# Kernel optimization log

Hardware: AMD Instinct MI355X
Metric: run time of the kernel (lower is better)

## Reference

```python
import jax, jax.numpy as jnp
import numpy as np

N = 50000      # nodes
E = 800000     # edges
F_NODE = 64
PE = 16
F_EDGE = 16
H = 128        # hidden_dim
L = 4          # num_layers
G = 64         # graphs in batch
NC = 10        # num_classes
BN_EPS = 1e-5


def _bn(h, g, b):
    # BatchNorm1d with batch statistics (deterministic train-style stats, no dropout)
    m = jnp.mean(h, axis=0)
    v = jnp.var(h, axis=0)
    return (h - m) * jax.lax.rsqrt(v + BN_EPS) * g + b


def setup_inputs() -> dict:
    key = jax.random.key(0)
    ks = jax.random.split(key, 16)
    p = lambda k, shape: (jax.random.normal(k, shape, jnp.float32) * 0.05)
    return dict(
        x=jax.random.normal(ks[0], (N, F_NODE), jnp.float32),
        pe=jax.random.normal(ks[1], (N, PE), jnp.float32),
        edge_index=jax.random.randint(ks[2], (2, E), 0, N),
        edge_attr=jax.random.normal(ks[3], (E, F_EDGE), jnp.float32),
        batch=jnp.sort(jax.random.randint(ks[4], (N,), 0, G)),
        W_in=p(ks[5], (F_NODE + PE, H)), b_in=jnp.zeros((H,), jnp.float32),
        We_edge=p(ks[6], (L, F_EDGE, H)), be_edge=jnp.zeros((L, H), jnp.float32),
        eps=jnp.zeros((L,), jnp.float32),
        W1_gin=p(ks[7], (L, H, 2 * H)), b1_gin=jnp.zeros((L, 2 * H), jnp.float32),
        W2_gin=p(ks[8], (L, 2 * H, H)), b2_gin=jnp.zeros((L, H), jnp.float32),
        bn1_g=jnp.ones((L, H), jnp.float32), bn1_b=jnp.zeros((L, H), jnp.float32),
        W1_ffn=p(ks[9], (L, H, 2 * H)), b1_ffn=jnp.zeros((L, 2 * H), jnp.float32),
        W2_ffn=p(ks[10], (L, 2 * H, H)), b2_ffn=jnp.zeros((L, H), jnp.float32),
        bn2_g=jnp.ones((L, H), jnp.float32), bn2_b=jnp.zeros((L, H), jnp.float32),
        W_r1=p(ks[11], (H, H)), b_r1=jnp.zeros((H,), jnp.float32),
        W_r2=p(ks[12], (H, NC)), b_r2=jnp.zeros((NC,), jnp.float32),
    )


def reference(x, pe, edge_index, edge_attr, batch,
              W_in, b_in, We_edge, be_edge, eps,
              W1_gin, b1_gin, W2_gin, b2_gin, bn1_g, bn1_b,
              W1_ffn, b1_ffn, W2_ffn, b2_ffn, bn2_g, bn2_b,
              W_r1, b_r1, W_r2, b_r2):
    src, dst = edge_index[0], edge_index[1]  # PyG: row=source j, col=target i
    # input projection on [x || pe]
    h = jax.nn.relu(jnp.concatenate([x, pe], axis=-1) @ W_in + b_in)  # [N,H]
    for l in range(L):
        # --- GINEConv: msg = relu(x_j + lin_edge(e_ij)); sum-aggregate to target
        e = edge_attr @ We_edge[l] + be_edge[l]                        # [E,H]
        msg = jax.nn.relu(h[src] + e)                                  # gather + fuse
        agg = jax.ops.segment_sum(msg, dst, num_segments=N)           # scatter-add
        z = (1.0 + eps[l]) * h + agg
        z = jax.nn.relu(z @ W1_gin[l] + b1_gin[l]) @ W2_gin[l] + b2_gin[l]
        # --- GNNPlusLayer: BN -> ReLU -> residual (identity proj, in==out)
        z = jax.nn.relu(_bn(z, bn1_g[l], bn1_b[l]))
        z = z + h
        # --- FFN (eval mode): out = lin2(relu(lin1(z))) + z, then BN
        f = jax.nn.relu(z @ W1_ffn[l] + b1_ffn[l]) @ W2_ffn[l] + b2_ffn[l]
        h = _bn(f + z, bn2_g[l], bn2_b[l])
    # --- global mean pool over graphs
    sums = jax.ops.segment_sum(h, batch, num_segments=G)               # [G,H]
    counts = jax.ops.segment_sum(jnp.ones((N,), h.dtype), batch, num_segments=G)
    hg = sums / jnp.maximum(counts, 1.0)[:, None]
    # --- readout MLP (dropout off in eval)
    return jax.nn.relu(hg @ W_r1 + b_r1) @ W_r2 + b_r2                 # [G,NC]
```

## Files before the change

kernel.cpp:

```cpp
#include <hip/hip_runtime.h>
#include <hip/hip_bf16.h>

#define NN 50000
#define NE 800000
#define FIN 80
#define H 128
#define H2 256
#define NG 64
#define NCLS 10
#define BN_EPS 1e-5f
#define NB 196
#define LDK 40
#define LDY 264

typedef __attribute__((ext_vector_type(8))) short bf16x8;
typedef __attribute__((ext_vector_type(8))) unsigned short us8;
typedef __attribute__((ext_vector_type(4))) float f32x4;
typedef __attribute__((ext_vector_type(2))) float f32x2;

__device__ __forceinline__ unsigned short f2b(float f) {
    __hip_bfloat16 h = __float2bfloat16(f);
    return *(unsigned short*)&h;
}
__device__ __forceinline__ float b2f(unsigned short u) {
    unsigned v = (unsigned)u << 16;
    return __uint_as_float(v);
}

__global__ void wprep_all(const float* __restrict__ W1g, const float* __restrict__ W2g,
                          const float* __restrict__ W1f, const float* __restrict__ W2f,
                          unsigned short* __restrict__ wt)
{
    const int idx = blockIdx.x * 256 + threadIdx.x;
    const int m = idx >> 17;
    const int r = idx & 131071;
    const float* W;
    unsigned short* Wt;
    int K, Nn;
    if (m == 0)      { W = W1g; Wt = wt;              K = 128; Nn = 256; }
    else if (m == 1) { W = W2g; Wt = wt + 4 * 65536;  K = 256; Nn = 128; }
    else if (m == 2) { W = W1f; Wt = wt + 8 * 65536;  K = 128; Nn = 256; }
    else             { W = W2f; Wt = wt + 12 * 65536; K = 256; Nn = 128; }
    const int per = K * Nn;
    const int l = r / per;
    const int rr = r - l * per;
    const int k = rr / Nn;
    const int n = rr - k * Nn;
    const float wv = W[r];
    const unsigned short hi = f2b(wv);
    const unsigned short lo = f2b(wv - b2f(hi));
    const int KB = K >> 5;
    const int kb = k >> 5, kk = k & 31;
    unsigned short* base = Wt + (size_t)l * 2 * per;
    base[((size_t)(0 * KB + kb) * Nn + n) * 32 + kk] = hi;
    base[((size_t)(1 * KB + kb) * Nn + n) * 32 + kk] = lo;
}

template<bool ZF>
__global__ __launch_bounds__(256, 2)
void gemm_pair(const void* __restrict__ Ap, const float* __restrict__ hres,
               const unsigned short* __restrict__ Wt1, const unsigned short* __restrict__ Wt2,
               const float* __restrict__ b1, const float* __restrict__ b2,
               const float* __restrict__ statsIn, const float* __restrict__ bng,
               const float* __restrict__ bnb, float* __restrict__ statsOut,
               float* __restrict__ Cout, float inv_n, int M)
{
    __shared__ unsigned short sA[ZF ? 128 : 1][LDK];
    __shared__ unsigned short sy[128][LDY];
    __shared__ float sAB[128];
    __shared__ float sSH[128];

    const int tid = threadIdx.x;
    const int m0 = blockIdx.x * 128;
    const int lane = tid & 63;
    const int w = tid >> 6;
    const int fr = lane & 15;
    const int fq = (lane >> 4) * 8;
    const int crow4 = (lane >> 4) * 4;

    if (ZF) {
#pragma unroll
        for (int rep = 0; rep < 2; ++rep) {
            const int c = lane + rep * 64;
            float su = 0.f, qu = 0.f;
#pragma unroll
            for (int s = 0; s < 8; ++s) {
                su += statsIn[s * 256 + c];
                qu += statsIn[s * 256 + 128 + c];
            }
            const float mean = su * inv_n;
            const float var = qu * inv_n - mean * mean;
            const float a = bng[c] * rsqrtf(var + BN_EPS);
            sAB[c] = a;
            sSH[c] = fmaf(-mean, a, bnb[c]);
        }
    }

    f32x4 acc1[2][16];
#pragma unroll
    for (int r = 0; r < 2; ++r)
#pragma unroll
        for (int c = 0; c < 16; ++c) acc1[r][c] = (f32x4)(0.f);

    const int arow = tid >> 1;
    const int akh = (tid & 1) * 16;
    const int gm = m0 + arow;

    for (int kb = 0; kb < 4; ++kb) {
        bf16x8 a0, a1;
        if (ZF) {
            if (gm < M) {
                const float* tf = (const float*)Ap + (size_t)gm * 128 + kb * 32 + akh;
                const float* hf = hres + (size_t)gm * 128 + kb * 32 + akh;
                const float4 t0 = *(const float4*)tf;
                const float4 t1 = *(const float4*)(tf + 4);
                const float4 t2 = *(const float4*)(tf + 8);
                const float4 t3 = *(const float4*)(tf + 12);
                const float4 h0 = *(const float4*)hf;
                const float4 h1 = *(const float4*)(hf + 4);
                const float4 h2 = *(const float4*)(hf + 8);
                const float4 h3 = *(const float4*)(hf + 12);
                const float tv[16] = {t0.x, t0.y, t0.z, t0.w, t1.x, t1.y, t1.z, t1.w,
                                      t2.x, t2.y, t2.z, t2.w, t3.x, t3.y, t3.z, t3.w};
                const float hv[16] = {h0.x, h0.y, h0.z, h0.w, h1.x, h1.y, h1.z, h1.w,
                                      h2.x, h2.y, h2.z, h2.w, h3.x, h3.y, h3.z, h3.w};
                us8 p0, p1;
#pragma unroll
                for (int i = 0; i < 8; ++i) {
                    const int c = kb * 32 + akh + i;
                    const int c2 = c + 8;
                    p0[i] = f2b(fmaxf(fmaf(tv[i], sAB[c], sSH[c]), 0.f) + hv[i]);
                    p1[i] = f2b(fmaxf(fmaf(tv[8 + i], sAB[c2], sSH[c2]), 0.f) + hv[8 + i]);
                }
                *(us8*)&sA[arow][akh]     = p0;
                *(us8*)&sA[arow][akh + 8] = p1;
            } else {
                *(float4*)&sA[arow][akh]     = make_float4(0.f, 0.f, 0.f, 0.f);
                *(float4*)&sA[arow][akh + 8] = make_float4(0.f, 0.f, 0.f, 0.f);
            }
            a0 = *(const bf16x8*)&sA[w * 32 + fr][kb * 32 + akh - akh + fq];
            a0 = *(const bf16x8*)&sA[w * 32 + fr][fq];
            a1 = *(const bf16x8*)&sA[w * 32 + 16 + fr][fq];
        } else {
            const unsigned short* z0 = (const unsigned short*)Ap +
                                       (size_t)(m0 + w * 32 + fr) * 128 + kb * 32 + fq;
            const unsigned short* z1 = (const unsigned short*)Ap +
                                       (size_t)(m0 + w * 32 + 16 + fr) * 128 + kb * 32 + fq;
            a0 = *(const bf16x8*)z0;
            a1 = *(const bf16x8*)z1;
        }
#pragma unroll
        for (int nt = 0; nt < 16; ++nt) {
            const bf16x8 bh = *(const bf16x8*)&Wt1[((size_t)(kb) * 256 + nt * 16 + fr) * 32 + fq];
            const bf16x8 bl = *(const bf16x8*)&Wt1[((size_t)(4 + kb) * 256 + nt * 16 + fr) * 32 + fq];
            acc1[0][nt] = __builtin_amdgcn_mfma_f32_16x16x32_bf16(a0, bh, acc1[0][nt], 0, 0, 0);
            acc1[0][nt] = __builtin_amdgcn_mfma_f32_16x16x32_bf16(a0, bl, acc1[0][nt], 0, 0, 0);
            acc1[1][nt] = __builtin_amdgcn_mfma_f32_16x16x32_bf16(a1, bh, acc1[1][nt], 0, 0, 0);
            acc1[1][nt] = __builtin_amdgcn_mfma_f32_16x16x32_bf16(a1, bl, acc1[1][nt], 0, 0, 0);
        }
    }

#pragma unroll
    for (int nt = 0; nt < 16; ++nt) {
        const float bb = b1[nt * 16 + fr];
#pragma unroll
        for (int r = 0; r < 2; ++r) {
            const int row0 = w * 32 + r * 16 + crow4;
#pragma unroll
            for (int reg = 0; reg < 4; ++reg) {
                const float o = fmaxf(acc1[r][nt][reg] + bb, 0.f);
                sy[row0 + reg][nt * 16 + fr] = f2b(o);
            }
        }
    }

    f32x4 acc2[2][8];
#pragma unroll
    for (int r = 0; r < 2; ++r)
#pragma unroll
        for (int c = 0; c < 8; ++c) acc2[r][c] = (f32x4)(0.f);

    for (int kb = 0; kb < 8; ++kb) {
        const bf16x8 ya0 = *(const bf16x8*)&sy[w * 32 + fr][kb * 32 + fq];
        const bf16x8 ya1 = *(const bf16x8*)&sy[w * 32 + 16 + fr][kb * 32 + fq];
#pragma unroll
        for (int ct = 0; ct < 8; ++ct) {
            const bf16x8 bh = *(const bf16x8*)&Wt2[((size_t)(kb) * 128 + ct * 16 + fr) * 32 + fq];
            const bf16x8 bl = *(const bf16x8*)&Wt2[((size_t)(8 + kb) * 128 + ct * 16 + fr) * 32 + fq];
            acc2[0][ct] = __builtin_amdgcn_mfma_f32_16x16x32_bf16(ya0, bh, acc2[0][ct], 0, 0, 0);
            acc2[0][ct] = __builtin_amdgcn_mfma_f32_16x16x32_bf16(ya0, bl, acc2[0][ct], 0, 0, 0);
            acc2[1][ct] = __builtin_amdgcn_mfma_f32_16x16x32_bf16(ya1, bh, acc2[1][ct], 0, 0, 0);
            acc2[1][ct] = __builtin_amdgcn_mfma_f32_16x16x32_bf16(ya1, bl, acc2[1][ct], 0, 0, 0);
        }
    }

    float s[8], q[8];
#pragma unroll
    for (int c = 0; c < 8; ++c) { s[c] = 0.f; q[c] = 0.f; }
#pragma unroll
    for (int r = 0; r < 2; ++r) {
        const int rbase = m0 + w * 32 + r * 16 + crow4;
#pragma unroll
        for (int ct = 0; ct < 8; ++ct) {
            const int gc = ct * 16 + fr;
            const float bb = b2[gc];
#pragma unroll
            for (int reg = 0; reg < 4; ++reg) {
                const int gr = rbase + reg;
                if (gr >= M) continue;
                float o = acc2[r][ct][reg] + bb;
                if (ZF) {
                    const float tv = ((const float*)Ap)[(size_t)gr * 128 + gc];
                    const float hv = hres[(size_t)gr * 128 + gc];
                    o += fmaxf(fmaf(tv, sAB[gc], sSH[gc]), 0.f) + hv;
                }
                s[ct] += o;
                q[ct] = fmaf(o, o, q[ct]);
                Cout[(size_t)gr * 128 + gc] = o;
            }
        }
    }

#pragma unroll
    for (int c = 0; c < 8; ++c) {
        s[c] += __shfl_xor(s[c], 32, 64); s[c] += __shfl_xor(s[c], 16, 64);
        q[c] += __shfl_xor(q[c], 32, 64); q[c] += __shfl_xor(q[c], 16, 64);
    }
    __syncthreads();
    float* red = (float*)sy;
    if (lane < 16) {
#pragma unroll
        for (int c = 0; c < 8; ++c) {
            red[w * 128 + c * 16 + lane]       = s[c];
            red[512 + w * 128 + c * 16 + lane] = q[c];
        }
    }
    __syncthreads();
    if (tid < 128) {
        const float ss = red[tid] + red[128 + tid] + red[256 + tid] + red[384 + tid];
        const float qq = red[512 + tid] + red[640 + tid] + red[768 + tid] + red[896 + tid];
        float* slab = statsOut + (blockIdx.x & 7) * 256;
        atomicAdd(&slab[tid], ss);
        atomicAdd(&slab[128 + tid], qq);
    }
}

__global__ __launch_bounds__(256, 4)
void inproj_kernel(const float* __restrict__ x, const float* __restrict__ pe,
                   const float* __restrict__ W, const float* __restrict__ bias,
                   float* __restrict__ C, unsigned short* __restrict__ Cb, int M)
{
    __shared__ float aT[16][129];
    __shared__ float wsh[16][129];

    const int tid = threadIdx.x;
    const int m0 = blockIdx.x * 128;
    const int rm = (tid >> 4) * 8;
    const int rn = (tid & 15) * 8;

    float acc[8][8];
#pragma unroll
    for (int i = 0; i < 8; ++i)
#pragma unroll
        for (int j = 0; j < 8; ++j) acc[i][j] = 0.f;

    const int lm = tid & 127;
    const int kq = (tid >> 7) * 8;
    const int wk = tid >> 4;
    const int wj = (tid & 15) * 8;

    for (int k0 = 0; k0 < FIN; k0 += 16) {
        {
            const int gm = m0 + lm;
            const int c = k0 + kq;
            if (gm < M) {
                const float* srcp = (c < 64) ? (x + (size_t)gm * 64 + c)
                                             : (pe + (size_t)gm * 16 + (c - 64));
                const float4 v0 = *(const float4*)srcp;
                const float4 v1 = *(const float4*)(srcp + 4);
                aT[kq + 0][lm] = v0.x; aT[kq + 1][lm] = v0.y;
                aT[kq + 2][lm] = v0.z; aT[kq + 3][lm] = v0.w;
                aT[kq + 4][lm] = v1.x; aT[kq + 5][lm] = v1.y;
                aT[kq + 6][lm] = v1.z; aT[kq + 7][lm] = v1.w;
            } else {
#pragma unroll
                for (int i = 0; i < 8; ++i) aT[kq + i][lm] = 0.f;
            }
        }
        {
#pragma unroll
            for (int j = 0; j < 8; ++j)
                wsh[wk][wj + j] = W[(size_t)(k0 + wk) * H + wj + j];
        }
        __syncthreads();
#pragma unroll
        for (int k = 0; k < 16; ++k) {
            const float av[8] = {aT[k][rm], aT[k][rm + 1], aT[k][rm + 2], aT[k][rm + 3],
                                 aT[k][rm + 4], aT[k][rm + 5], aT[k][rm + 6], aT[k][rm + 7]};
            const float bv[8] = {wsh[k][rn], wsh[k][rn + 1], wsh[k][rn + 2], wsh[k][rn + 3],
                                 wsh[k][rn + 4], wsh[k][rn + 5], wsh[k][rn + 6], wsh[k][rn + 7]};
#pragma unroll
            for (int i = 0; i < 8; ++i)
#pragma unroll
                for (int j = 0; j < 8; ++j)
                    acc[i][j] = fmaf(av[i], bv[j], acc[i][j]);
        }
        __syncthreads();
    }

    float bv[8];
#pragma unroll
    for (int j = 0; j < 8; ++j) bv[j] = bias[rn + j];
#pragma unroll
    for (int i = 0; i < 8; ++i) {
        const int gm = m0 + rm + i;
        if (gm >= M) continue;
        float o[8];
#pragma unroll
        for (int j = 0; j < 8; ++j) o[j] = fmaxf(acc[i][j] + bv[j], 0.f);
        *(float4*)&C[(size_t)gm * H + rn]     = make_float4(o[0], o[1], o[2], o[3]);
        *(float4*)&C[(size_t)gm * H + rn + 4] = make_float4(o[4], o[5], o[6], o[7]);
        us8 pk;
#pragma unroll
        for (int j = 0; j < 8; ++j) pk[j] = f2b(o[j]);
        *(us8*)&Cb[(size_t)gm * H + rn] = pk;
    }
}

__global__ void hist_kernel(const int* __restrict__ ei, int* __restrict__ deg)
{
    const int e = blockIdx.x * 256 + threadIdx.x;
    if (e < NE) atomicAdd(&deg[ei[NE + e]], 1);
}

__global__ void bsum_kernel(const int* __restrict__ deg, int* __restrict__ bsum)
{
    const int tid = threadIdx.x;
    const int i = blockIdx.x * 256 + tid;
    int v = (i < NN) ? deg[i] : 0;
#pragma unroll
    for (int off = 32; off > 0; off >>= 1) v += __shfl_down(v, off, 64);
    __shared__ int ws[4];
    if ((tid & 63) == 0) ws[tid >> 6] = v;
    __syncthreads();
    if (tid == 0) bsum[blockIdx.x] = ws[0] + ws[1] + ws[2] + ws[3];
}

__global__ void bscan_kernel(int* __restrict__ bsum)
{
    __shared__ int sh[256];
    const int tid = threadIdx.x;
    sh[tid] = (tid < NB) ? bsum[tid] : 0;
    __syncthreads();
    for (int off = 1; off < 256; off <<= 1) {
        const int t = (tid >= off) ? sh[tid - off] : 0;
        __syncthreads();
        sh[tid] += t;
        __syncthreads();
    }
    if (tid < NB) bsum[tid] = (tid == 0) ? 0 : sh[tid - 1];
}

__global__ void bwrite_kernel(const int* __restrict__ deg, const int* __restrict__ boff,
                              int* __restrict__ rowptr, int* __restrict__ cursor)
{
    __shared__ int sh[256];
    const int tid = threadIdx.x;
    const int i = blockIdx.x * 256 + tid;
    const int v = (i < NN) ? deg[i] : 0;
    sh[tid] = v;
    __syncthreads();
    for (int off = 1; off < 256; off <<= 1) {
        const int t = (tid >= off) ? sh[tid - off] : 0;
        __syncthreads();
        sh[tid] += t;
        __syncthreads();
    }
    if (i < NN) {
        const int pos = boff[blockIdx.x] + sh[tid] - v;
        rowptr[i] = pos;
        cursor[i] = pos;
    }
    if (blockIdx.x == 0 && tid == 0) rowptr[NN] = NE;
}

__global__ void scat_idx(const int* __restrict__ ei, int* __restrict__ cursor,
                         int* __restrict__ src_s, int* __restrict__ perm)
{
    const int e = blockIdx.x * 256 + threadIdx.x;
    if (e >= NE) return;
    const int pos = atomicAdd(&cursor[ei[NE + e]], 1);
    src_s[pos] = ei[e];
    perm[pos] = e;
}

__global__ void gather_ea(const float* __restrict__ ea, const int* __restrict__ perm,
                          float* __restrict__ ea_s)
{
    const int idx = blockIdx.x * 256 + threadIdx.x;
    const int pos = idx >> 2;
    const int qd = idx & 3;
    const int e = perm[pos];
    *(float4*)&ea_s[(size_t)pos * 16 + qd * 4] = *(const float4*)&ea[(size_t)e * 16 + qd * 4];
}

__global__ __launch_bounds__(256)
void agg_kernel(const float* __restrict__ h, const unsigned short* __restrict__ hb,
                const int* __restrict__ rowptr, const int* __restrict__ src_s,
                const float* __restrict__ ea_s, const float* __restrict__ We,
                const float* __restrict__ be, const float* __restrict__ eps, int l,
                unsigned short* __restrict__ zb)
{
    const int lane = threadIdx.x & 63;
    const int w = threadIdx.x >> 6;
    const int n = blockIdx.x * 4 + w;
    if (n >= NN) return;

    f32x2 wv[16];
#pragma unroll
    for (int k = 0; k < 16; ++k)
        wv[k] = *(const f32x2*)&We[k * H + 2 * lane];
    const f32x2 bev = *(const f32x2*)&be[2 * lane];

    const int beg = __builtin_amdgcn_readfirstlane(rowptr[n]);
    const int end = __builtin_amdgcn_readfirstlane(rowptr[n + 1]);

    const float e1 = 1.0f + eps[l];
    f32x2 acc = (*(const f32x2*)&h[(size_t)n * H + 2 * lane]) * e1;

    for (int i0 = beg; i0 < end; i0 += 16) {
        const int jn = min(16, end - i0);
        int srcs[16];
#pragma unroll
        for (int j = 0; j < 16; ++j)
            srcs[j] = src_s[(i0 + j < end) ? (i0 + j) : (end - 1)];
        unsigned hraw[16];
#pragma unroll
        for (int j = 0; j < 16; ++j)
            hraw[j] = *(const unsigned*)&hb[(size_t)srcs[j] * H + 2 * lane];
#pragma unroll
        for (int j = 0; j < 16; ++j) {
            if (j >= jn) break;
            const float* ar = ea_s + (size_t)(i0 + j) * 16;
            f32x2 s2 = bev;
#pragma unroll
            for (int k = 0; k < 16; ++k)
                s2 = __builtin_elementwise_fma((f32x2)(ar[k]), wv[k], s2);
            f32x2 hv = {__uint_as_float(hraw[j] << 16),
                        __uint_as_float(hraw[j] & 0xffff0000u)};
            f32x2 m = hv + s2;
            m = __builtin_elementwise_max(m, (f32x2)(0.f));
            acc += m;
        }
    }
    const unsigned u = ((unsigned)f2b(acc[1]) << 16) | (unsigned)f2b(acc[0]);
    *(unsigned*)&zb[(size_t)n * H + 2 * lane] = u;
}

__global__ void bn_apply_kernel(const float* __restrict__ u, const float* __restrict__ st,
                                const float* __restrict__ g, const float* __restrict__ b,
                                float* __restrict__ h, unsigned short* __restrict__ hb,
                                float inv_n)
{
    const int i = blockIdx.x * 256 + threadIdx.x;
    const int c = i & (H - 1);
    float su = 0.f, qu = 0.f;
#pragma unroll
    for (int s = 0; s < 8; ++s) { su += st[s * 256 + c]; qu += st[s * 256 + 128 + c]; }
    const float mean = su * inv_n;
    const float var = qu * inv_n - mean * mean;
    const float a = g[c] * rsqrtf(var + BN_EPS);
    const float sh = fmaf(-mean, a, b[c]);
    const float v = fmaf(u[i], a, sh);
    h[i] = v;
    hb[i] = f2b(v);
}

__global__ void pool_kernel(const float* __restrict__ h, const int* __restrict__ batch,
                            float* __restrict__ pool, float* __restrict__ cnt, int n)
{
    const int c = threadIdx.x & (H - 1);
    const int half = threadIdx.x >> 7;
    const int r0 = blockIdx.x * 256 + half * 128;
    if (r0 >= n) return;
    const int rend = min(r0 + 128, n);
    int gprev = batch[r0];
    float acc = 0.f;
    int run = 0;
    for (int r = r0; r < rend; ++r) {
        const int g = batch[r];
        if (g != gprev) {
            atomicAdd(&pool[gprev * H + c], acc);
            if (c == 0) atomicAdd(&cnt[gprev], (float)run);
            acc = 0.f; run = 0; gprev = g;
        }
        acc += h[(size_t)r * H + c];
        run++;
    }
    atomicAdd(&pool[gprev * H + c], acc);
    if (c == 0) atomicAdd(&cnt[gprev], (float)run);
}

__global__ void readout_kernel(const float* __restrict__ pool, const float* __restrict__ cnt,
                               const float* __restrict__ Wr1, const float* __restrict__ br1,
                               const float* __restrict__ Wr2, const float* __restrict__ br2,
                               float* __restrict__ out)
{
    __shared__ float hg[H];
    __shared__ float r1[H];
    const int g = blockIdx.x;
    const int j = threadIdx.x;
    hg[j] = pool[g * H + j] / fmaxf(cnt[g], 1.0f);
    __syncthreads();
    float acc = br1[j];
    for (int k = 0; k < H; ++k) acc = fmaf(hg[k], Wr1[k * H + j], acc);
    r1[j] = fmaxf(acc, 0.f);
    __syncthreads();
    if (j < NCLS) {
        float o = br2[j];
        for (int k = 0; k < H; ++k) o = fmaf(r1[k], Wr2[k * NCLS + j], o);
        out[g * NCLS + j] = o;
    }
}

extern "C" void kernel_launch(void* const* d_in, const int* in_sizes, int n_in,
                              void* d_out, int out_size, void* d_ws, size_t ws_size,
                              hipStream_t stream)
{
    const float* x       = (const float*)d_in[0];
    const float* pe      = (const float*)d_in[1];
    const int*   ei      = (const int*)d_in[2];
    const float* ea      = (const float*)d_in[3];
    const int*   batch   = (const int*)d_in[4];
    const float* W_in    = (const float*)d_in[5];
    const float* b_in    = (const float*)d_in[6];
    const float* We_edge = (const float*)d_in[7];
    const float* be_edge = (const float*)d_in[8];
    const float* eps     = (const float*)d_in[9];
    const float* W1g     = (const float*)d_in[10];
    const float* b1g     = (const float*)d_in[11];
    const float* W2g     = (const float*)d_in[12];
    const float* b2g     = (const float*)d_in[13];
    const float* bn1g    = (const float*)d_in[14];
    const float* bn1b    = (const float*)d_in[15];
    const float* W1f     = (const float*)d_in[16];
    const float* b1f     = (const float*)d_in[17];
    const float* W2f     = (const float*)d_in[18];
    const float* b2f     = (const float*)d_in[19];
    const float* bn2g    = (const float*)d_in[20];
    const float* bn2b    = (const float*)d_in[21];
    const float* Wr1     = (const float*)d_in[22];
    const float* br1     = (const float*)d_in[23];
    const float* Wr2     = (const float*)d_in[24];
    const float* br2     = (const float*)d_in[25];
    float* out = (float*)d_out;

    const size_t NH = (size_t)NN * H;
    float* hbuf  = (float*)d_ws;
    float* tbuf  = hbuf + NH;
    unsigned short* zb = (unsigned short*)(tbuf + NH);
    int*   perm  = (int*)(zb + NH);
    int*   deg   = perm + NE;
    float* stats = (float*)(deg + NN);
    float* pool  = stats + 16384;
    float* cnt   = pool + NG * H;
    int*   rowptr = (int*)(cnt + NG);
    int*   cursor = rowptr + NN + 1;
    int*   bsum   = cursor + NN;
    int*   src_s  = bsum + 256;
    float* ea_s   = (float*)(src_s + NE);
    unsigned short* hb = (unsigned short*)(ea_s + (size_t)NE * 16);
    unsigned short* wt = hb + NH;
    unsigned short* wt1g = wt;
    unsigned short* wt2g = wt + 4 * 65536;
    unsigned short* wt1f = wt + 8 * 65536;
    unsigned short* wt2f = wt + 12 * 65536;

    const dim3 blk(256);
    const dim3 ip_g((NN + 127) / 128, 1);
    const dim3 gp_g((NN + 127) / 128, 1);
    const int ew_grid = (int)(NH / 256);
    const float inv_n = 1.0f / (float)NN;
    const size_t zero_bytes = (size_t)(NN + 16384 + NG * H + NG) * 4;

    wprep_all<<<2048, blk, 0, stream>>>(W1g, W2g, W1f, W2f, wt);

    hipMemsetAsync(deg, 0, zero_bytes, stream);
    hist_kernel<<<(NE + 255) / 256, blk, 0, stream>>>(ei, deg);
    bsum_kernel<<<NB, blk, 0, stream>>>(deg, bsum);
    bscan_kernel<<<1, blk, 0, stream>>>(bsum);
    bwrite_kernel<<<NB, blk, 0, stream>>>(deg, bsum, rowptr, cursor);
    scat_idx<<<(NE + 255) / 256, blk, 0, stream>>>(ei, cursor, src_s, perm);
    gather_ea<<<(NE * 4) / 256, blk, 0, stream>>>(ea, perm, ea_s);

    inproj_kernel<<<ip_g, blk, 0, stream>>>(x, pe, W_in, b_in, hbuf, hb, NN);

    for (int l = 0; l < 4; ++l) {
        float* s1 = stats + (size_t)l * 4096;
        float* s2 = s1 + 2048;

        agg_kernel<<<(NN + 3) / 4, blk, 0, stream>>>(hbuf, hb, rowptr, src_s, ea_s,
                                                     We_edge + (size_t)l * 16 * H,
                                                     be_edge + (size_t)l * H, eps, l, zb);

        gemm_pair<false><<<gp_g, blk, 0, stream>>>(
            zb, nullptr, wt1g + (size_t)l * 65536, wt2g + (size_t)l * 65536,
            b1g + (size_t)l * H2, b2g + (size_t)l * H,
            nullptr, nullptr, nullptr, s1, tbuf, inv_n, NN);

        gemm_pair<true><<<gp_g, blk, 0, stream>>>(
            tbuf, hbuf, wt1f + (size_t)l * 65536, wt2f + (size_t)l * 65536,
            b1f + (size_t)l * H2, b2f + (size_t)l * H,
            s1, bn1g + (size_t)l * H, bn1b + (size_t)l * H, s2, tbuf, inv_n, NN);

        bn_apply_kernel<<<ew_grid, blk, 0, stream>>>(tbuf, s2, bn2g + (size_t)l * H,
                                                     bn2b + (size_t)l * H, hbuf, hb, inv_n);
    }

    pool_kernel<<<(NN + 255) / 256, blk, 0, stream>>>(hbuf, batch, pool, cnt, NN);
    readout_kernel<<<NG, H, 0, stream>>>(pool, cnt, Wr1, br1, Wr2, br2, out);
}
```

Measured before the change: 1.145 ms.

## Split fused MLP hidden dim into halves and aggregate two nodes per wavefront

The fused two-GEMM kernel now computes the 256-wide hidden layer in two 128-column halves and feeds each half straight into the second GEMM. This halves the first-stage accumulator registers and the hidden-activation LDS buffer, which should raise occupancy. A-operand fragments are kept in registers and reused for the second half. The edge aggregation kernel now has each wavefront process two destination nodes at once, interleaving their gathers to expose more memory-level parallelism, at the cost of more registers and imbalance when the two node degrees differ.

```diff
diff --git a/kernel.cpp b/kernel.cpp
--- a/kernel.cpp
+++ b/kernel.cpp
@@ -11,7 +11,7 @@
 #define BN_EPS 1e-5f
 #define NB 196
 #define LDK 40
-#define LDY 264
+#define LDY 136
 
 typedef __attribute__((ext_vector_type(8))) short bf16x8;
 typedef __attribute__((ext_vector_type(8))) unsigned short us8;
@@ -96,101 +96,112 @@
         }
     }
 
-    f32x4 acc1[2][16];
-#pragma unroll
-    for (int r = 0; r < 2; ++r)
-#pragma unroll
-        for (int c = 0; c < 16; ++c) acc1[r][c] = (f32x4)(0.f);
-
     const int arow = tid >> 1;
     const int akh = (tid & 1) * 16;
     const int gm = m0 + arow;
 
-    for (int kb = 0; kb < 4; ++kb) {
-        bf16x8 a0, a1;
-        if (ZF) {
-            if (gm < M) {
-                const float* tf = (const float*)Ap + (size_t)gm * 128 + kb * 32 + akh;
-                const float* hf = hres + (size_t)gm * 128 + kb * 32 + akh;
-                const float4 t0 = *(const float4*)tf;
-                const float4 t1 = *(const float4*)(tf + 4);
-                const float4 t2 = *(const float4*)(tf + 8);
-                const float4 t3 = *(const float4*)(tf + 12);
-                const float4 h0 = *(const float4*)hf;
-                const float4 h1 = *(const float4*)(hf + 4);
-                const float4 h2 = *(const float4*)(hf + 8);
-                const float4 h3 = *(const float4*)(hf + 12);
-                const float tv[16] = {t0.x, t0.y, t0.z, t0.w, t1.x, t1.y, t1.z, t1.w,
-                                      t2.x, t2.y, t2.z, t2.w, t3.x, t3.y, t3.z, t3.w};
-                const float hv[16] = {h0.x, h0.y, h0.z, h0.w, h1.x, h1.y, h1.z, h1.w,
-                                      h2.x, h2.y, h2.z, h2.w, h3.x, h3.y, h3.z, h3.w};
-                us8 p0, p1;
-#pragma unroll
-                for (int i = 0; i < 8; ++i) {
-                    const int c = kb * 32 + akh + i;
-                    const int c2 = c + 8;
-                    p0[i] = f2b(fmaxf(fmaf(tv[i], sAB[c], sSH[c]), 0.f) + hv[i]);
-                    p1[i] = f2b(fmaxf(fmaf(tv[8 + i], sAB[c2], sSH[c2]), 0.f) + hv[8 + i]);
+    bf16x8 ac[2][4];
+    f32x4 acc2[2][8];
+#pragma unroll
+    for (int r = 0; r < 2; ++r)
+#pragma unroll
+        for (int c = 0; c < 8; ++c) acc2[r][c] = (f32x4)(0.f);
+
+    for (int h2 = 0; h2 < 2; ++h2) {
+        f32x4 acc1[2][8];
+#pragma unroll
+        for (int r = 0; r < 2; ++r)
+#pragma unroll
+            for (int c = 0; c < 8; ++c) acc1[r][c] = (f32x4)(0.f);
+
+        for (int kb = 0; kb < 4; ++kb) {
+            bf16x8 a0, a1;
+            if (h2 == 0) {
+                if (ZF) {
+                    if (gm < M) {
+                        const float* tf = (const float*)Ap + (size_t)gm * 128 + kb * 32 + akh;
+                        const float* hf = hres + (size_t)gm * 128 + kb * 32 + akh;
+                        const float4 t0 = *(const float4*)tf;
+                        const float4 t1 = *(const float4*)(tf + 4);
+                        const float4 t2 = *(const float4*)(tf + 8);
+                        const float4 t3 = *(const float4*)(tf + 12);
+                        const float4 h0 = *(const float4*)hf;
+                        const float4 h1 = *(const float4*)(hf + 4);
+                        const float4 h2v = *(const float4*)(hf + 8);
+                        const float4 h3 = *(const float4*)(hf + 12);
+                        const float tv[16] = {t0.x, t0.y, t0.z, t0.w, t1.x, t1.y, t1.z, t1.w,
+                                              t2.x, t2.y, t2.z, t2.w, t3.x, t3.y, t3.z, t3.w};
+                        const float hv[16] = {h0.x, h0.y, h0.z, h0.w, h1.x, h1.y, h1.z, h1.w,
+                                              h2v.x, h2v.y, h2v.z, h2v.w, h3.x, h3.y, h3.z, h3.w};
+                        us8 p0, p1;
+#pragma unroll
+                        for (int i = 0; i < 8; ++i) {
+                            const int c = kb * 32 + akh + i;
+                            const int c2 = c + 8;
+                            p0[i] = f2b(fmaxf(fmaf(tv[i], sAB[c], sSH[c]), 0.f) + hv[i]);
+                            p1[i] = f2b(fmaxf(fmaf(tv[8 + i], sAB[c2], sSH[c2]), 0.f) + hv[8 + i]);
+                        }
+                        *(us8*)&sA[arow][akh]     = p0;
+                        *(us8*)&sA[arow][akh + 8] = p1;
+                    } else {
+                        *(float4*)&sA[arow][akh]     = make_float4(0.f, 0.f, 0.f, 0.f);
+                        *(float4*)&sA[arow][akh + 8] = make_float4(0.f, 0.f, 0.f, 0.f);
+                    }
+                    a0 = *(const bf16x8*)&sA[w * 32 + fr][fq];
+                    a1 = *(const bf16x8*)&sA[w * 32 + 16 + fr][fq];
+                } else {
+                    const unsigned short* z0 = (const unsigned short*)Ap +
+                                               (size_t)(m0 + w * 32 + fr) * 128 + kb * 32 + fq;
+                    const unsigned short* z1 = (const unsigned short*)Ap +
+                                               (size_t)(m0 + w * 32 + 16 + fr) * 128 + kb * 32 + fq;
+                    a0 = *(const bf16x8*)z0;
+                    a1 = *(const bf16x8*)z1;
                 }
-                *(us8*)&sA[arow][akh]     = p0;
-                *(us8*)&sA[arow][akh + 8] = p1;
+                ac[0][kb] = a0;
+                ac[1][kb] = a1;
             } else {
-                *(float4*)&sA[arow][akh]     = make_float4(0.f, 0.f, 0.f, 0.f);
-                *(float4*)&sA[arow][akh + 8] = make_float4(0.f, 0.f, 0.f, 0.f);
+                a0 = ac[0][kb];
+                a1 = ac[1][kb];
             }
-            a0 = *(const bf16x8*)&sA[w * 32 + fr][kb * 32 + akh - akh + fq];
-            a0 = *(const bf16x8*)&sA[w * 32 + fr][fq];
-            a1 = *(const bf16x8*)&sA[w * 32 + 16 + fr][fq];
-        } else {
-            const unsigned short* z0 = (const unsigned short*)Ap +
-                                       (size_t)(m0 + w * 32 + fr) * 128 + kb * 32 + fq;
-            const unsigned short* z1 = (const unsigned short*)Ap +
-                                       (size_t)(m0 + w * 32 + 16 + fr) * 128 + kb * 32 + fq;
-            a0 = *(const bf16x8*)z0;
-            a1 = *(const bf16x8*)z1;
-        }
-#pragma unroll
-        for (int nt = 0; nt < 16; ++nt) {
-            const bf16x8 bh = *(const bf16x8*)&Wt1[((size_t)(kb) * 256 + nt * 16 + fr) * 32 + fq];
-            const bf16x8 bl = *(const bf16x8*)&Wt1[((size_t)(4 + kb) * 256 + nt * 16 + fr) * 32 + fq];
-            acc1[0][nt] = __builtin_amdgcn_mfma_f32_16x16x32_bf16(a0, bh, acc1[0][nt], 0, 0, 0);
-            acc1[0][nt] = __builtin_amdgcn_mfma_f32_16x16x32_bf16(a0, bl, acc1[0][nt], 0, 0, 0);
-            acc1[1][nt] = __builtin_amdgcn_mfma_f32_16x16x32_bf16(a1, bh, acc1[1][nt], 0, 0, 0);
-            acc1[1][nt] = __builtin_amdgcn_mfma_f32_16x16x32_bf16(a1, bl, acc1[1][nt], 0, 0, 0);
-        }
-    }
-
-#pragma unroll
-    for (int nt = 0; nt < 16; ++nt) {
-        const float bb = b1[nt * 16 + fr];
-#pragma unroll
-        for (int r = 0; r < 2; ++r) {
-            const int row0 = w * 32 + r * 16 + crow4;
-#pragma unroll
-            for (int reg = 0; reg < 4; ++reg) {
-                const float o = fmaxf(acc1[r][nt][reg] + bb, 0.f);
-                sy[row0 + reg][nt * 16 + fr] = f2b(o);
+#pragma unroll
+            for (int nt = 0; nt < 8; ++nt) {
+                const int nrow = h2 * 128 + nt * 16 + fr;
+                const bf16x8 bh = *(const bf16x8*)&Wt1[((size_t)(kb) * 256 + nrow) * 32 + fq];
+                const bf16x8 bl = *(const bf16x8*)&Wt1[((size_t)(4 + kb) * 256 + nrow) * 32 + fq];
+                acc1[0][nt] = __builtin_amdgcn_mfma_f32_16x16x32_bf16(a0, bh, acc1[0][nt], 0, 0, 0);
+                acc1[0][nt] = __builtin_amdgcn_mfma_f32_16x16x32_bf16(a0, bl, acc1[0][nt], 0, 0, 0);
+                acc1[1][nt] = __builtin_amdgcn_mfma_f32_16x16x32_bf16(a1, bh, acc1[1][nt], 0, 0, 0);
+                acc1[1][nt] = __builtin_amdgcn_mfma_f32_16x16x32_bf16(a1, bl, acc1[1][nt], 0, 0, 0);
             }
         }
-    }
-
-    f32x4 acc2[2][8];
-#pragma unroll
-    for (int r = 0; r < 2; ++r)
-#pragma unroll
-        for (int c = 0; c < 8; ++c) acc2[r][c] = (f32x4)(0.f);
-
-    for (int kb = 0; kb < 8; ++kb) {
-        const bf16x8 ya0 = *(const bf16x8*)&sy[w * 32 + fr][kb * 32 + fq];
-        const bf16x8 ya1 = *(const bf16x8*)&sy[w * 32 + 16 + fr][kb * 32 + fq];
-#pragma unroll
-        for (int ct = 0; ct < 8; ++ct) {
-            const bf16x8 bh = *(const bf16x8*)&Wt2[((size_t)(kb) * 128 + ct * 16 + fr) * 32 + fq];
-            const bf16x8 bl = *(const bf16x8*)&Wt2[((size_t)(8 + kb) * 128 + ct * 16 + fr) * 32 + fq];
-            acc2[0][ct] = __builtin_amdgcn_mfma_f32_16x16x32_bf16(ya0, bh, acc2[0][ct], 0, 0, 0);
-            acc2[0][ct] = __builtin_amdgcn_mfma_f32_16x16x32_bf16(ya0, bl, acc2[0][ct], 0, 0, 0);
-            acc2[1][ct] = __builtin_amdgcn_mfma_f32_16x16x32_bf16(ya1, bh, acc2[1][ct], 0, 0, 0);
-            acc2[1][ct] = __builtin_amdgcn_mfma_f32_16x16x32_bf16(ya1, bl, acc2[1][ct], 0, 0, 0);
+
+#pragma unroll
+        for (int nt = 0; nt < 8; ++nt) {
+            const float bb = b1[h2 * 128 + nt * 16 + fr];
+#pragma unroll
+            for (int r = 0; r < 2; ++r) {
+                const int row0 = w * 32 + r * 16 + crow4;
+#pragma unroll
+                for (int reg = 0; reg < 4; ++reg) {
+                    const float o = fmaxf(acc1[r][nt][reg] + bb, 0.f);
+                    sy[row0 + reg][nt * 16 + fr] = f2b(o);
+                }
+            }
+        }
+
+        for (int kb2 = 0; kb2 < 4; ++kb2) {
+            const bf16x8 ya0 = *(const bf16x8*)&sy[w * 32 + fr][kb2 * 32 + fq];
+            const bf16x8 ya1 = *(const bf16x8*)&sy[w * 32 + 16 + fr][kb2 * 32 + fq];
+            const int kg = h2 * 4 + kb2;
+#pragma unroll
+            for (int ct = 0; ct < 8; ++ct) {
+                const bf16x8 bh = *(const bf16x8*)&Wt2[((size_t)(kg) * 128 + ct * 16 + fr) * 32 + fq];
+                const bf16x8 bl = *(const bf16x8*)&Wt2[((size_t)(8 + kg) * 128 + ct * 16 + fr) * 32 + fq];
+                acc2[0][ct] = __builtin_amdgcn_mfma_f32_16x16x32_bf16(ya0, bh, acc2[0][ct], 0, 0, 0);
+                acc2[0][ct] = __builtin_amdgcn_mfma_f32_16x16x32_bf16(ya0, bl, acc2[0][ct], 0, 0, 0);
+                acc2[1][ct] = __builtin_amdgcn_mfma_f32_16x16x32_bf16(ya1, bh, acc2[1][ct], 0, 0, 0);
+                acc2[1][ct] = __builtin_amdgcn_mfma_f32_16x16x32_bf16(ya1, bl, acc2[1][ct], 0, 0, 0);
+            }
         }
     }
 
@@ -413,8 +424,10 @@
 {
     const int lane = threadIdx.x & 63;
     const int w = threadIdx.x >> 6;
-    const int n = blockIdx.x * 4 + w;
-    if (n >= NN) return;
+    const int n0 = blockIdx.x * 8 + w * 2;
+    if (n0 >= NN) return;
+    const bool has1 = (n0 + 1 < NN);
+    const int n1 = has1 ? (n0 + 1) : n0;
 
     f32x2 wv[16];
 #pragma unroll
@@ -422,39 +435,72 @@
         wv[k] = *(const f32x2*)&We[k * H + 2 * lane];
     const f32x2 bev = *(const f32x2*)&be[2 * lane];
 
-    const int beg = __builtin_amdgcn_readfirstlane(rowptr[n]);
-    const int end = __builtin_amdgcn_readfirstlane(rowptr[n + 1]);
+    const int beg0 = __builtin_amdgcn_readfirstlane(rowptr[n0]);
+    const int end0 = __builtin_amdgcn_readfirstlane(rowptr[n0 + 1]);
+    const int beg1 = __builtin_amdgcn_readfirstlane(rowptr[n1]);
+    const int end1 = __builtin_amdgcn_readfirstlane(rowptr[n1 + 1]);
 
     const float e1 = 1.0f + eps[l];
-    f32x2 acc = (*(const f32x2*)&h[(size_t)n * H + 2 * lane]) * e1;
-
-    for (int i0 = beg; i0 < end; i0 += 16) {
-        const int jn = min(16, end - i0);
-        int srcs[16];
+    f32x2 acc0 = (*(const f32x2*)&h[(size_t)n0 * H + 2 * lane]) * e1;
+    f32x2 acc1 = (*(const f32x2*)&h[(size_t)n1 * H + 2 * lane]) * e1;
+
+    int i0 = beg0, i1 = beg1;
+    while (i0 < end0 || i1 < end1) {
+        const int jn0 = min(16, end0 - i0);
+        const int jn1 = has1 ? min(16, end1 - i1) : 0;
+        int s0[16], s1[16];
+#pragma unroll
+        for (int j = 0; j < 16; ++j) {
+            s0[j] = src_s[min(i0 + ((j < jn0) ? j : 0), NE - 1)];
+            s1[j] = src_s[min(i1 + ((j < jn1) ? j : 0), NE - 1)];
+        }
+        unsigned hr0[16], hr1[16];
 #pragma unroll
         for (int j = 0; j < 16; ++j)
-            srcs[j] = src_s[(i0 + j < end) ? (i0 + j) : (end - 1)];
-        unsigned hraw[16];
+            hr0[j] = *(const unsigned*)&hb[(size_t)s0[j] * H + 2 * lane];
 #pragma unroll
         for (int j = 0; j < 16; ++j)
-            hraw[j] = *(const unsigned*)&hb[(size_t)srcs[j] * H + 2 * lane];
+            hr1[j] = *(const unsigned*)&hb[(size_t)s1[j] * H + 2 * lane];
+
 #pragma unroll
         for (int j = 0; j < 16; ++j) {
-            if (j >= jn) break;
+            if (j >= jn0) break;
             const float* ar = ea_s + (size_t)(i0 + j) * 16;
             f32x2 s2 = bev;
 #pragma unroll
             for (int k = 0; k < 16; ++k)
                 s2 = __builtin_elementwise_fma((f32x2)(ar[k]), wv[k], s2);
-            f32x2 hv = {__uint_as_float(hraw[j] << 16),
-                        __uint_as_float(hraw[j] & 0xffff0000u)};
+            f32x2 hv = {__uint_as_float(hr0[j] << 16),
+                        __uint_as_float(hr0[j] & 0xffff0000u)};
             f32x2 m = hv + s2;
             m = __builtin_elementwise_max(m, (f32x2)(0.f));
-            acc += m;
-        }
-    }
-    const unsigned u = ((unsigned)f2b(acc[1]) << 16) | (unsigned)f2b(acc[0]);
-    *(unsigned*)&zb[(size_t)n * H + 2 * lane] = u;
+            acc0 += m;
+        }
+#pragma unroll
+        for (int j = 0; j < 16; ++j) {
+            if (j >= jn1) break;
+            const float* ar = ea_s + (size_t)(i1 + j) * 16;
+            f32x2 s2 = bev;
+#pragma unroll
+            for (int k = 0; k < 16; ++k)
+                s2 = __builtin_elementwise_fma((f32x2)(ar[k]), wv[k], s2);
+            f32x2 hv = {__uint_as_float(hr1[j] << 16),
+                        __uint_as_float(hr1[j] & 0xffff0000u)};
+            f32x2 m = hv + s2;
+            m = __builtin_elementwise_max(m, (f32x2)(0.f));
+            acc1 += m;
+        }
+        if (jn0 > 0) i0 += jn0;
+        if (jn1 > 0) i1 += jn1;
+    }
+    {
+        const unsigned u = ((unsigned)f2b(acc0[1]) << 16) | (unsigned)f2b(acc0[0]);
+        *(unsigned*)&zb[(size_t)n0 * H + 2 * lane] = u;
+    }
+    if (has1) {
+        const unsigned u = ((unsigned)f2b(acc1[1]) << 16) | (unsigned)f2b(acc1[0]);
+        *(unsigned*)&zb[(size_t)n1 * H + 2 * lane] = u;
+    }
 }
 
 __global__ void bn_apply_kernel(const float* __restrict__ u, const float* __restrict__ st,
@@ -599,7 +645,7 @@
         float* s1 = stats + (size_t)l * 4096;
         float* s2 = s1 + 2048;
 
-        agg_kernel<<<(NN + 3) / 4, blk, 0, stream>>>(hbuf, hb, rowptr, src_s, ea_s,
+        agg_kernel<<<(NN + 7) / 8, blk, 0, stream>>>(hbuf, hb, rowptr, src_s, ea_s,
                                                      We_edge + (size_t)l * 16 * H,
                                                      be_edge + (size_t)l * H, eps, l, zb);
 
```

New measurement: 1.489 ms. +30.0%, slower.
